# Kernel tuning notes

Hardware: AMD Instinct MI355X
Metric: run time of the kernel (lower is better)

The kernel has to match this reference:

```python
import jax, jax.numpy as jnp
import numpy as np

D = 1024
POOL_SIZES = [1024, 512, 256, 128, 64]  # n_pos=32*32 -> n_codes=64
CODEBOOK_SIZE = 512
BATCH = 32
W_SCALE = 0.03125  # ~1/sqrt(D) so pre-softmax logits stay O(1)


def setup_inputs() -> dict:
    key = jax.random.key(0)
    ks = jax.random.split(key, 7)
    x = jax.random.normal(ks[0], (BATCH, POOL_SIZES[0], D), dtype=jnp.float32)
    queries = jax.random.normal(ks[1], (len(POOL_SIZES), POOL_SIZES[0], D), dtype=jnp.float32)
    wq = jax.random.normal(ks[2], (len(POOL_SIZES), D, D), dtype=jnp.float32) * W_SCALE
    wk = jax.random.normal(ks[3], (len(POOL_SIZES), D, D), dtype=jnp.float32) * W_SCALE
    wv = jax.random.normal(ks[4], (len(POOL_SIZES), D, D), dtype=jnp.float32) * W_SCALE
    wo = jax.random.normal(ks[5], (len(POOL_SIZES), D, D), dtype=jnp.float32) * W_SCALE
    codebook = jax.random.normal(ks[6], (CODEBOOK_SIZE, D), dtype=jnp.float32)
    return {"x": x, "queries": queries, "wq": wq, "wk": wk, "wv": wv, "wo": wo, "codebook": codebook}


def reference(x, queries, wq, wk, wv, wo, codebook):
    # StackedPooling: S -> 1024 -> 512 -> 256 -> 128 -> 64 via AttentionPool stages
    scale = D ** (-0.5)
    h = x
    for i, K in enumerate(POOL_SIZES):
        q = queries[i, :K, :] @ wq[i]              # [K, D] learned queries, q_proj
        k = jnp.einsum("bsd,de->bse", h, wk[i])    # [B, S, D]
        v = jnp.einsum("bsd,de->bse", h, wv[i])    # [B, S, D]
        logits = jnp.einsum("kd,bsd->bks", q, k) * scale
        attn = jax.nn.softmax(logits, axis=-1)     # [B, K, S]
        pooled = jnp.einsum("bks,bsd->bkd", attn, v)
        h = jnp.einsum("bkd,de->bke", pooled, wo[i])  # [B, K, D]
    # VQ codebook quantization: nearest code per latent (squared L2)
    z = h                                          # [B, n_codes, D]
    d2 = (jnp.sum(z * z, axis=-1, keepdims=True)
          - 2.0 * jnp.einsum("bkd,cd->bkc", z, codebook)
          + jnp.sum(codebook * codebook, axis=-1))  # [B, n_codes, C]
    idx = jnp.argmin(d2, axis=-1)                  # [B, n_codes] int
    z_q = codebook[idx]                            # [B, n_codes, D]
    # straight-through estimator
    out = z + jax.lax.stop_gradient(z_q - z)
    return out
```

## Files before the change

### kernel.cpp

```cpp
#include <hip/hip_runtime.h>


#define MB (1024ull * 1024ull)

typedef unsigned short u16;
typedef __attribute__((ext_vector_type(4))) float f32x4;
typedef __bf16 bf16x8 __attribute__((ext_vector_type(8)));

__device__ __forceinline__ u16 f2bf(float f) {
  unsigned u = __float_as_uint(f);
  unsigned r = u + 0x7FFFu + ((u >> 16) & 1u);
  return (u16)(r >> 16);
}
__device__ __forceinline__ float bf2f(u16 h) {
  return __uint_as_float(((unsigned)h) << 16);
}

typedef __attribute__((address_space(1))) const void GASV;
typedef __attribute__((address_space(3))) void LASV;
__device__ __forceinline__ void async16(const void* g, void* l) {
  __builtin_amdgcn_global_load_lds((GASV*)g, (LASV*)l, 16, 0, 0);
}

__device__ __forceinline__ int xcd_swz(int bid, int nwg) {
  const int q8 = nwg >> 3, r8 = nwg & 7;
  const int xcd = bid & 7, idx = bid >> 3;
  return (xcd < r8 ? xcd * (q8 + 1) : r8 * (q8 + 1) + (xcd - r8) * q8) + idx;
}

template<int MODE>
__global__ __launch_bounds__(512, 1)
void gemm_c(const u16* __restrict__ A, const u16* __restrict__ B,
            float* __restrict__ Cf, u16* __restrict__ Cb,
            int M, int N, int KLEN, int ld,
            long long sA, long long sB, long long sC, int ldc, float alpha,
            int nxt, int nyt)
{
  __shared__ u16 lds[65536];
  const int tid  = threadIdx.x;
  const int lane = tid & 63;
  const int w    = tid >> 6;
  const int wr   = w >> 2, wc = w & 3;

  const int wg = xcd_swz((int)blockIdx.x, (int)gridDim.x);
  const int bx = wg % nxt;
  const int by = (wg / nxt) % nyt;
  const int bz = wg / (nxt * nyt);

  const int m0 = by * 256, n0 = bx * 256;
  const u16* Ab = A + (size_t)bz * sA;
  const u16* Bb = B + (size_t)bz * sB;
  const int NT = KLEN >> 6;

  f32x4 acc[8][4] = {};

  const int Rl  = tid >> 2;
  const int sgs = (tid & 3) ^ ((tid >> 3) & 3);
  int ra0 = m0 + Rl;        ra0 = ra0 < M - 1 ? ra0 : M - 1;
  int ra1 = m0 + 128 + Rl;  ra1 = ra1 < M - 1 ? ra1 : M - 1;
  int rb0 = n0 + Rl;        rb0 = rb0 < N - 1 ? rb0 : N - 1;
  int rb1 = n0 + 128 + Rl;  rb1 = rb1 < N - 1 ? rb1 : N - 1;
  const u16* gA0 = Ab + (size_t)ra0 * ld + (sgs << 3);
  const u16* gA1 = Ab + (size_t)ra1 * ld + (sgs << 3);
  const u16* gB0 = Bb + (size_t)rb0 * ld + (sgs << 3);
  const u16* gB1 = Bb + (size_t)rb1 * ld + (sgs << 3);
  const int ldst = (w << 4) * 32;

  auto stageH = [&](int mat, int buf, int kh, int tile) {
    const int tt = tile < NT ? tile : NT - 1;
    const int kc = (tt << 6) + (kh << 5);
    u16* d = &lds[(mat << 15) + (buf << 14) + (kh << 13) + ldst];
    if (mat == 0) {
      async16(gA0 + kc, d);
      async16(gA1 + kc, d + 4096);
    } else {
      async16(gB0 + kc, d);
      async16(gB1 + kc, d + 4096);
    }
  };

  const int rsel = lane & 15;
  const int ksub = lane >> 4;
  const int sw   = ksub ^ ((rsel >> 1) & 3);
  const u16* ldsA = &lds[(wr * 128 + rsel) * 32 + sw * 8];
  const u16* ldsB = &lds[32768 + (wc * 64 + rsel) * 32 + sw * 8];

  auto phase = [&](int buf, int kh, int mh, bf16x8* b,
                   int smat, int sbuf, int skh, int stile, int vm) {
    bf16x8 a[4];
    if (mh == 0) {
#pragma unroll
      for (int ni = 0; ni < 4; ++ni)
        b[ni] = *(const bf16x8*)&ldsB[buf * 16384 + kh * 8192 + ni * 512];
    }
#pragma unroll
    for (int mi = 0; mi < 4; ++mi)
      a[mi] = *(const bf16x8*)&ldsA[buf * 16384 + kh * 8192 + mh * 2048 + mi * 512];
    stageH(smat, sbuf, skh, stile);
    if (vm == 10)     asm volatile("s_waitcnt vmcnt(10)" ::: "memory");
    else if (vm == 6) asm volatile("s_waitcnt vmcnt(6)" ::: "memory");
    __builtin_amdgcn_s_barrier();
    asm volatile("s_waitcnt lgkmcnt(0)" ::: "memory");
    __builtin_amdgcn_sched_barrier(0);
    __builtin_amdgcn_s_setprio(1);
#pragma unroll
    for (int mi = 0; mi < 4; ++mi)
#pragma unroll
      for (int ni = 0; ni < 4; ++ni)
        acc[mh * 4 + mi][ni] = __builtin_amdgcn_mfma_f32_16x16x32_bf16(
            a[mi], b[ni], acc[mh * 4 + mi][ni], 0, 0, 0);
    __builtin_amdgcn_s_setprio(0);
    __builtin_amdgcn_s_barrier();
  };

  stageH(1, 0, 0, 0); stageH(0, 0, 0, 0); stageH(1, 0, 1, 0); stageH(0, 0, 1, 0);
  stageH(1, 1, 0, 1); stageH(0, 1, 0, 1); stageH(1, 1, 1, 1);
  asm volatile("s_waitcnt vmcnt(6)" ::: "memory");
  __builtin_amdgcn_s_barrier();

  const int NI = NT >> 1;
  for (int it = 0; it < NI; ++it) {
    const int t0 = it << 1, t1 = t0 + 1;
    bf16x8 b0[4], b1[4];
    phase(0, 0, 0, b0, 0, 1, 1, t1,     -1);
    phase(0, 0, 1, b0, 1, 0, 0, t0 + 2, -1);
    phase(0, 1, 0, b1, 0, 0, 0, t0 + 2, -1);
    phase(0, 1, 1, b1, 1, 0, 1, t0 + 2, 10);
    phase(1, 0, 0, b0, 0, 0, 1, t0 + 2, -1);
    phase(1, 0, 1, b0, 1, 1, 0, t1 + 2, 10);
    phase(1, 1, 0, b1, 0, 1, 0, t1 + 2, -1);
    phase(1, 1, 1, b1, 1, 1, 1, t1 + 2, 6);
  }
  asm volatile("s_waitcnt vmcnt(0)" ::: "memory");

#pragma unroll
  for (int mi = 0; mi < 8; ++mi)
#pragma unroll
    for (int ni = 0; ni < 4; ++ni)
#pragma unroll
      for (int i = 0; i < 4; ++i) {
        const int row = m0 + wr * 128 + mi * 16 + ((lane >> 4) << 2) + i;
        const int col = n0 + wc * 64 + ni * 16 + rsel;
        if (row < M && col < N) {
          const float v = acc[mi][ni][i] * alpha;
          const size_t off = (size_t)bz * sC + (size_t)row * ldc + col;
          if (MODE == 0) Cf[off] = v;
          else           Cb[off] = f2bf(v);
        }
      }
}

template<int MODE>
__global__ __launch_bounds__(256, 2)
void gemm_s(const u16* __restrict__ A, const u16* __restrict__ B,
            float* __restrict__ Cf, u16* __restrict__ Cb,
            int M, int N, int KLEN, int ld,
            long long sA, long long sB, long long sC, int ldc, float alpha,
            int nxt, int nyt)
{
  __shared__ u16 lds[32768];
  const int tid  = threadIdx.x;
  const int lane = tid & 63;
  const int w    = tid >> 6;
  const int wr   = w >> 1, wc = w & 1;

  const int wg = xcd_swz((int)blockIdx.x, (int)gridDim.x);
  const int bx = wg % nxt;
  const int by = (wg / nxt) % nyt;
  const int bz = wg / (nxt * nyt);

  const int m0 = by * 128, n0 = bx * 128;
  const u16* Ab = A + (size_t)bz * sA;
  const u16* Bb = B + (size_t)bz * sB;
  const int NT = KLEN >> 6;

  f32x4 acc[4][4] = {};

  const int Rl  = tid >> 3;
  const int sgs = (tid & 7) ^ (Rl & 7);
  const int ldst = (w << 3) * 64;

  auto stage = [&](int t, int buf) {
    const int kc = t << 6;
#pragma unroll
    for (int mat = 0; mat < 2; ++mat)
#pragma unroll
      for (int j = 0; j < 4; ++j) {
        int rg = (mat ? n0 : m0) + j * 32 + Rl;
        const int lim = (mat ? N : M) - 1;
        rg = rg < lim ? rg : lim;
        const u16* src = (mat ? Bb : Ab) + (size_t)rg * ld + kc + (sgs << 3);
        async16(src, &lds[(buf << 14) + (mat << 13) + j * 2048 + ldst]);
      }
  };

  const int rsel = lane & 15, ksub = lane >> 4;
  const int e  = rsel & 7;
  const int s0 = ((e >> 2) << 2) | (ksub ^ (e & 3));
  const int s1 = s0 ^ 4;
  const u16* ldsA0 = &lds[(wr * 64 + rsel) * 64 + s0 * 8];
  const u16* ldsA1 = &lds[(wr * 64 + rsel) * 64 + s1 * 8];
  const u16* ldsB0 = &lds[8192 + (wc * 64 + rsel) * 64 + s0 * 8];
  const u16* ldsB1 = &lds[8192 + (wc * 64 + rsel) * 64 + s1 * 8];

  stage(0, 0);
  for (int t = 0; t < NT; ++t) {
    const int buf = t & 1;
    if (t + 1 < NT) {
      stage(t + 1, buf ^ 1);
      asm volatile("s_waitcnt vmcnt(8)" ::: "memory");
    } else {
      asm volatile("s_waitcnt vmcnt(0)" ::: "memory");
    }
    __builtin_amdgcn_s_barrier();
    bf16x8 af[4][2], bf[4][2];
#pragma unroll
    for (int f = 0; f < 4; ++f) {
      af[f][0] = *(const bf16x8*)&ldsA0[buf * 16384 + f * 1024];
      af[f][1] = *(const bf16x8*)&ldsA1[buf * 16384 + f * 1024];
      bf[f][0] = *(const bf16x8*)&ldsB0[buf * 16384 + f * 1024];
      bf[f][1] = *(const bf16x8*)&ldsB1[buf * 16384 + f * 1024];
    }
    asm volatile("s_waitcnt lgkmcnt(0)" ::: "memory");
    __builtin_amdgcn_sched_barrier(0);
    __builtin_amdgcn_s_setprio(1);
#pragma unroll
    for (int mi = 0; mi < 4; ++mi)
#pragma unroll
      for (int ni = 0; ni < 4; ++ni)
#pragma unroll
        for (int kh = 0; kh < 2; ++kh)
          acc[mi][ni] = __builtin_amdgcn_mfma_f32_16x16x32_bf16(
              af[mi][kh], bf[ni][kh], acc[mi][ni], 0, 0, 0);
    __builtin_amdgcn_s_setprio(0);
    __builtin_amdgcn_s_barrier();
  }

#pragma unroll
  for (int mi = 0; mi < 4; ++mi)
#pragma unroll
    for (int ni = 0; ni < 4; ++ni)
#pragma unroll
      for (int i = 0; i < 4; ++i) {
        const int row = m0 + wr * 64 + mi * 16 + ((lane >> 4) << 2) + i;
        const int col = n0 + wc * 64 + ni * 16 + rsel;
        if (row < M && col < N) {
          const float v = acc[mi][ni][i] * alpha;
          const size_t off = (size_t)bz * sC + (size_t)row * ldc + col;
          if (MODE == 0) Cf[off] = v;
          else           Cb[off] = f2bf(v);
        }
      }
}

__global__ void cast_k(const float* __restrict__ in, u16* __restrict__ out,
                       long long n4)
{
  long long i = (long long)blockIdx.x * 256 + threadIdx.x;
  const long long stride = (long long)gridDim.x * 256;
  for (; i < n4; i += stride) {
    const float4 v = *(const float4*)&in[i << 2];
    *(ushort4*)&out[i << 2] = make_ushort4(f2bf(v.x), f2bf(v.y), f2bf(v.z), f2bf(v.w));
  }
}

__global__ __launch_bounds__(256)
void cast_trans_k(const float* __restrict__ in, u16* __restrict__ h,
                  u16* __restrict__ ht)
{
  __shared__ float t[32][33];
  const int z = blockIdx.z;
  const float* src = in + (size_t)z * 1048576;
  u16* dh = h  + (size_t)z * 1048576;
  u16* dt = ht + (size_t)z * 1048576;
  const int x0 = blockIdx.x * 32, y0 = blockIdx.y * 32;
  const int tx = threadIdx.x, ty = threadIdx.y;
#pragma unroll
  for (int k = 0; k < 4; ++k) {
    const float v = src[(size_t)(y0 + ty + 8 * k) * 1024 + (x0 + tx)];
    t[ty + 8 * k][tx] = v;
    dh[(size_t)(y0 + ty + 8 * k) * 1024 + (x0 + tx)] = f2bf(v);
  }
  __syncthreads();
#pragma unroll
  for (int k = 0; k < 4; ++k)
    dt[(size_t)(x0 + ty + 8 * k) * 1024 + (y0 + tx)] = f2bf(t[tx][ty + 8 * k]);
}

__global__ __launch_bounds__(256)
void transpose_cast_k(const float* __restrict__ in, u16* __restrict__ out)
{
  __shared__ float t[32][33];
  const int z = blockIdx.z;
  const float* src = in + (size_t)z * 1048576;
  u16* dst = out + (size_t)z * 1048576;
  const int x0 = blockIdx.x * 32, y0 = blockIdx.y * 32;
  const int tx = threadIdx.x, ty = threadIdx.y;
#pragma unroll
  for (int k = 0; k < 4; ++k)
    t[ty + 8 * k][tx] = src[(size_t)(y0 + ty + 8 * k) * 1024 + (x0 + tx)];
  __syncthreads();
#pragma unroll
  for (int k = 0; k < 4; ++k)
    dst[(size_t)(x0 + ty + 8 * k) * 1024 + (y0 + tx)] = f2bf(t[tx][ty + 8 * k]);
}

__global__ __launch_bounds__(256)
void transpose_u16_k(const u16* __restrict__ in, u16* __restrict__ out, int R)
{
  __shared__ u16 t[32][33];
  const size_t zi = (size_t)blockIdx.z * R * 1024;
  const size_t zo = (size_t)blockIdx.z * 1024 * R;
  const int x0 = blockIdx.x * 32, y0 = blockIdx.y * 32;
  const int tx = threadIdx.x, ty = threadIdx.y;
#pragma unroll
  for (int k = 0; k < 4; ++k)
    t[ty + 8 * k][tx] = in[zi + (size_t)(y0 + ty + 8 * k) * 1024 + (x0 + tx)];
  __syncthreads();
#pragma unroll
  for (int k = 0; k < 4; ++k)
    out[zo + (size_t)(x0 + ty + 8 * k) * R + (y0 + tx)] = t[tx][ty + 8 * k];
}

__global__ __launch_bounds__(256)
void softmax_b(const u16* __restrict__ lg, u16* __restrict__ at, int S)
{
  const size_t row = blockIdx.x;
  const u16* src = lg + row * S;
  const int tid = threadIdx.x;
  float v[4];
  float mx = -3.402823466e38f;
#pragma unroll
  for (int c = 0; c < 4; ++c) {
    const int j = tid + c * 256;
    v[c] = (j < S) ? bf2f(src[j]) : -3.402823466e38f;
    mx = fmaxf(mx, v[c]);
  }
#pragma unroll
  for (int o = 32; o > 0; o >>= 1) mx = fmaxf(mx, __shfl_xor(mx, o));
  __shared__ float rmx[4];
  if ((tid & 63) == 0) rmx[tid >> 6] = mx;
  __syncthreads();
  mx = fmaxf(fmaxf(rmx[0], rmx[1]), fmaxf(rmx[2], rmx[3]));
  float sum = 0.f;
#pragma unroll
  for (int c = 0; c < 4; ++c) { v[c] = expf(v[c] - mx); sum += v[c]; }
#pragma unroll
  for (int o = 32; o > 0; o >>= 1) sum += __shfl_xor(sum, o);
  __shared__ float rsm[4];
  if ((tid & 63) == 0) rsm[tid >> 6] = sum;
  __syncthreads();
  sum = rsm[0] + rsm[1] + rsm[2] + rsm[3];
  const float inv = 1.0f / sum;
  u16* dst = at + row * S;
#pragma unroll
  for (int c = 0; c < 4; ++c) {
    const int j = tid + c * 256;
    if (j < S) dst[j] = f2bf(v[c] * inv);
  }
}

__global__ __launch_bounds__(256)
void cnorm_kernel(const float* __restrict__ cb, float* __restrict__ cn)
{
  const int c = blockIdx.x;
  const float4 v = ((const float4*)(cb + (size_t)c * 1024))[threadIdx.x];
  float s = v.x * v.x + v.y * v.y + v.z * v.z + v.w * v.w;
#pragma unroll
  for (int o = 32; o > 0; o >>= 1) s += __shfl_xor(s, o);
  __shared__ float r4[4];
  if ((threadIdx.x & 63) == 0) r4[threadIdx.x >> 6] = s;
  __syncthreads();
  if (threadIdx.x == 0) cn[c] = r4[0] + r4[1] + r4[2] + r4[3];
}

__global__ __launch_bounds__(256)
void argmin_gather_k(const float* __restrict__ dot, const float* __restrict__ cn,
                     const float* __restrict__ cb, float* __restrict__ out)
{
  const size_t lat = blockIdx.x;
  const int tid = threadIdx.x;
  float best = 3.402823466e38f;
  int bi = 0;
#pragma unroll
  for (int cc = 0; cc < 2; ++cc) {
    const int c = tid + cc * 256;
    float d = 0.f;
#pragma unroll
    for (int p = 0; p < 4; ++p) d += dot[(size_t)p * 1048576 + lat * 512 + c];
    const float sc = cn[c] - 2.0f * d;
    if (sc < best || (sc == best && c < bi)) { best = sc; bi = c; }
  }
  __shared__ float rb[256];
  __shared__ int   ri[256];
  rb[tid] = best; ri[tid] = bi;
  __syncthreads();
  for (int s = 128; s > 0; s >>= 1) {
    if (tid < s) {
      const float ob = rb[tid + s];
      const int oi = ri[tid + s];
      if (ob < rb[tid] || (ob == rb[tid] && oi < ri[tid])) { rb[tid] = ob; ri[tid] = oi; }
    }
    __syncthreads();
  }
  const int sel = ri[0];
  ((float4*)(out + lat * 1024))[tid] = ((const float4*)(cb + (size_t)sel * 1024))[tid];
}

__global__ void fill_kernel(float* p, float v, int n) {
  const int i = blockIdx.x * 256 + threadIdx.x;
  if (i < n) p[i] = v;
}

static void gX(hipStream_t st, int mode,
               const u16* A, const u16* B, float* Cf, u16* Cb,
               int M, int N, int KLEN, int ld,
               long long sA, long long sB, long long sC, int ldc,
               int batch, float alpha)
{
  const int b256 = ((M + 255) / 256) * ((N + 255) / 256) * batch;
  if (b256 >= 192 && (KLEN & 127) == 0) {
    const int nxt = (N + 255) / 256, nyt = (M + 255) / 256;
    dim3 grid(nxt * nyt * batch), blk(512);
    if (mode == 0)
      gemm_c<0><<<grid, blk, 0, st>>>(A, B, Cf, Cb, M, N, KLEN, ld, sA, sB, sC, ldc, alpha, nxt, nyt);
    else
      gemm_c<1><<<grid, blk, 0, st>>>(A, B, Cf, Cb, M, N, KLEN, ld, sA, sB, sC, ldc, alpha, nxt, nyt);
  } else {
    const int nxt = (N + 127) / 128, nyt = (M + 127) / 128;
    dim3 grid(nxt * nyt * batch), blk(256);
    if (mode == 0)
      gemm_s<0><<<grid, blk, 0, st>>>(A, B, Cf, Cb, M, N, KLEN, ld, sA, sB, sC, ldc, alpha, nxt, nyt);
    else
      gemm_s<1><<<grid, blk, 0, st>>>(A, B, Cf, Cb, M, N, KLEN, ld, sA, sB, sC, ldc, alpha, nxt, nyt);
  }
}

extern "C" void kernel_launch(void* const* d_in, const int* in_sizes, int n_in,
                              void* d_out, int out_size, void* d_ws, size_t ws_size,
                              hipStream_t stream)
{
  const float* x   = (const float*)d_in[0];
  const float* qry = (const float*)d_in[1];
  const float* wq  = (const float*)d_in[2];
  const float* wk  = (const float*)d_in[3];
  const float* wv  = (const float*)d_in[4];
  const float* wo  = (const float*)d_in[5];
  const float* cb  = (const float*)d_in[6];
  float* out = (float*)d_out;

  const size_t NEED = 298 * MB;
  if (ws_size < NEED) {
    fill_kernel<<<(out_size + 255) / 256, 256, 0, stream>>>(out, (float)ws_size, out_size);
    return;
  }
  char* ws = (char*)d_ws;
  const long long W = 1048576;
  u16*  QKb  = (u16*)(ws + 0 * MB);
  u16*  WVOb = (u16*)(ws + 10 * MB);
  u16*  CBb  = (u16*)(ws + 20 * MB);
  float* CN  = (float*)(ws + 21 * MB);
  u16*  Zb   = (u16*)(ws + 22 * MB);
  float* DOT = (float*)(ws + 26 * MB);
  u16*  Hb   = (u16*)(ws + 42 * MB);
  u16*  HTb  = (u16*)(ws + 106 * MB);
  u16*  ATb  = (u16*)(ws + 170 * MB);
  u16*  LOG  = (u16*)(ws + 234 * MB);
  u16*  Mb   = (u16*)(ws + 234 * MB);
  u16*  QSb   = (u16*)(ws + 42 * MB);
  u16*  WQb   = (u16*)(ws + 52 * MB);
  u16*  WKb   = (u16*)(ws + 62 * MB);
  u16*  WVb   = (u16*)(ws + 72 * MB);
  u16*  WOTb  = (u16*)(ws + 82 * MB);
  u16*  WqkTb = (u16*)(ws + 92 * MB);

  const int S_in[5]  = {1024, 1024, 512, 256, 128};
  const int K_out[5] = {1024, 512, 256, 128, 64};

  cast_k<<<2048, 256, 0, stream>>>(qry, QSb, 1310720ll);
  cast_k<<<2048, 256, 0, stream>>>(wq, WQb, 1310720ll);
  cast_k<<<2048, 256, 0, stream>>>(wk, WKb, 1310720ll);
  cast_k<<<2048, 256, 0, stream>>>(wv, WVb, 1310720ll);
  cast_k<<<512, 256, 0, stream>>>(cb, CBb, 131072ll);
  dim3 tb(32, 8), tg5(32, 32, 5);
  transpose_cast_k<<<tg5, tb, 0, stream>>>(wo, WOTb);
  cnorm_kernel<<<512, 256, 0, stream>>>(cb, CN);

  gX(stream, 1, WKb, WQb, nullptr, WqkTb, 1024, 1024, 1024, 1024, W, W, W, 1024, 5, 1.0f);
  gX(stream, 1, QSb, WqkTb, nullptr, QKb, 1024, 1024, 1024, 1024, W, W, W, 1024, 5, 1.0f);
  gX(stream, 1, WOTb, WVb, nullptr, WVOb, 1024, 1024, 1024, 1024, W, W, W, 1024, 5, 1.0f);

  dim3 tgx(32, 32, 32);
  cast_trans_k<<<tgx, tb, 0, stream>>>(x, Hb, HTb);

  for (int i = 0; i < 5; ++i) {
    const int S = S_in[i], KO = K_out[i];

    gX(stream, 1, QKb + (size_t)i * W, Hb, nullptr, LOG,
       KO, S, 1024, 1024, 0, (long long)S * 1024, (long long)KO * S, S, 32, 0.03125f);
    softmax_b<<<32 * KO, 256, 0, stream>>>(LOG, ATb, S);
    gX(stream, 1, ATb, HTb, nullptr, Mb,
       KO, 1024, S, S, (long long)KO * S, (long long)1024 * S, (long long)KO * 1024, 1024, 32, 1.0f);
    if (i < 4) {
      gX(stream, 1, Mb, WVOb + (size_t)i * W, nullptr, Hb,
         32 * KO, 1024, 1024, 1024, 0, 0, 0, 1024, 1, 1.0f);
      dim3 tgt(32, KO / 32, 32);
      transpose_u16_k<<<tgt, tb, 0, stream>>>(Hb, HTb, KO);
    } else {
      gX(stream, 1, Mb, WVOb + (size_t)i * W, nullptr, Zb,
         32 * KO, 1024, 1024, 1024, 0, 0, 0, 1024, 1, 1.0f);
    }
  }

  gX(stream, 0, Zb, CBb, DOT, nullptr,
     2048, 512, 256, 1024, 256, 256, (long long)2048 * 512, 512, 4, 1.0f);
  argmin_gather_k<<<2048, 256, 0, stream>>>(DOT, CN, cb, out);
}
```

Measured before the change: 772.3 us.

## Fold per-stage value/output projections into query and codebook weight products

Result: faster. 733.1 us (-5.1%).

```diff
diff --git a/kernel.cpp b/kernel.cpp
--- a/kernel.cpp
+++ b/kernel.cpp
@@ -70,13 +70,8 @@
     const int tt = tile < NT ? tile : NT - 1;
     const int kc = (tt << 6) + (kh << 5);
     u16* d = &lds[(mat << 15) + (buf << 14) + (kh << 13) + ldst];
-    if (mat == 0) {
-      async16(gA0 + kc, d);
-      async16(gA1 + kc, d + 4096);
-    } else {
-      async16(gB0 + kc, d);
-      async16(gB1 + kc, d + 4096);
-    }
+    if (mat == 0) { async16(gA0 + kc, d); async16(gA1 + kc, d + 4096); }
+    else          { async16(gB0 + kc, d); async16(gB1 + kc, d + 4096); }
   };
 
   const int rsel = lane & 15;
@@ -380,15 +375,13 @@
 {
   const size_t lat = blockIdx.x;
   const int tid = threadIdx.x;
+  const float* dr = dot + lat * 512;
   float best = 3.402823466e38f;
   int bi = 0;
 #pragma unroll
   for (int cc = 0; cc < 2; ++cc) {
     const int c = tid + cc * 256;
-    float d = 0.f;
-#pragma unroll
-    for (int p = 0; p < 4; ++p) d += dot[(size_t)p * 1048576 + lat * 512 + c];
-    const float sc = cn[c] - 2.0f * d;
+    const float sc = cn[c] - 2.0f * dr[c];
     if (sc < best || (sc == best && c < bi)) { best = sc; bi = c; }
   }
   __shared__ float rb[256];
@@ -412,14 +405,15 @@
   if (i < n) p[i] = v;
 }
 
-static void gX(hipStream_t st, int mode,
+static void gX(hipStream_t st, int mode, int force,
                const u16* A, const u16* B, float* Cf, u16* Cb,
                int M, int N, int KLEN, int ld,
                long long sA, long long sB, long long sC, int ldc,
                int batch, float alpha)
 {
   const int b256 = ((M + 255) / 256) * ((N + 255) / 256) * batch;
-  if (b256 >= 192 && (KLEN & 127) == 0) {
+  const bool big = (force == 2) || (force == 0 && b256 >= 192 && (KLEN & 127) == 0);
+  if (big) {
     const int nxt = (N + 255) / 256, nyt = (M + 255) / 256;
     dim3 grid(nxt * nyt * batch), blk(512);
     if (mode == 0)
@@ -449,7 +443,7 @@
   const float* cb  = (const float*)d_in[6];
   float* out = (float*)d_out;
 
-  const size_t NEED = 298 * MB;
+  const size_t NEED = 312 * MB;
   if (ws_size < NEED) {
     fill_kernel<<<(out_size + 255) / 256, 256, 0, stream>>>(out, (float)ws_size, out_size);
     return;
@@ -458,21 +452,24 @@
   const long long W = 1048576;
   u16*  QKb  = (u16*)(ws + 0 * MB);
   u16*  WVOb = (u16*)(ws + 10 * MB);
-  u16*  CBb  = (u16*)(ws + 20 * MB);
-  float* CN  = (float*)(ws + 21 * MB);
-  u16*  Zb   = (u16*)(ws + 22 * MB);
-  float* DOT = (float*)(ws + 26 * MB);
-  u16*  Hb   = (u16*)(ws + 42 * MB);
-  u16*  HTb  = (u16*)(ws + 106 * MB);
-  u16*  ATb  = (u16*)(ws + 170 * MB);
-  u16*  LOG  = (u16*)(ws + 234 * MB);
-  u16*  Mb   = (u16*)(ws + 234 * MB);
-  u16*  QSb   = (u16*)(ws + 42 * MB);
-  u16*  WQb   = (u16*)(ws + 52 * MB);
-  u16*  WKb   = (u16*)(ws + 62 * MB);
-  u16*  WVb   = (u16*)(ws + 72 * MB);
-  u16*  WOTb  = (u16*)(ws + 82 * MB);
-  u16*  WqkTb = (u16*)(ws + 92 * MB);
+  u16*  WVOs = (u16*)(ws + 20 * MB);
+  u16*  CBb  = (u16*)(ws + 30 * MB);
+  float* CN  = (float*)(ws + 31 * MB);
+  u16*  QKP  = (u16*)(ws + 32 * MB);
+  u16*  WCb  = (u16*)(ws + 40 * MB);
+  u16*  WC5  = (u16*)(ws + 48 * MB);
+  u16*  CBW  = (u16*)(ws + 50 * MB);
+  float* DOT = (float*)(ws + 51 * MB);
+  u16*  U    = (u16*)(ws + 56 * MB);
+  u16*  UT   = (u16*)(ws + 120 * MB);
+  u16*  ATb  = (u16*)(ws + 184 * MB);
+  u16*  LOG  = (u16*)(ws + 248 * MB);
+  u16*  QSb   = (u16*)(ws + 56 * MB);
+  u16*  WQb   = (u16*)(ws + 66 * MB);
+  u16*  WKb   = (u16*)(ws + 76 * MB);
+  u16*  WVb   = (u16*)(ws + 86 * MB);
+  u16*  WOTb  = (u16*)(ws + 96 * MB);
+  u16*  WqkTb = (u16*)(ws + 106 * MB);
 
   const int S_in[5]  = {1024, 1024, 512, 256, 128};
   const int K_out[5] = {1024, 512, 256, 128, 64};
@@ -486,33 +483,38 @@
   transpose_cast_k<<<tg5, tb, 0, stream>>>(wo, WOTb);
   cnorm_kernel<<<512, 256, 0, stream>>>(cb, CN);
 
-  gX(stream, 1, WKb, WQb, nullptr, WqkTb, 1024, 1024, 1024, 1024, W, W, W, 1024, 5, 1.0f);
-  gX(stream, 1, QSb, WqkTb, nullptr, QKb, 1024, 1024, 1024, 1024, W, W, W, 1024, 5, 1.0f);
-  gX(stream, 1, WOTb, WVb, nullptr, WVOb, 1024, 1024, 1024, 1024, W, W, W, 1024, 5, 1.0f);
+  gX(stream, 1, 0, WKb, WQb, nullptr, WqkTb, 1024, 1024, 1024, 1024, W, W, W, 1024, 5, 1.0f);
+  gX(stream, 1, 0, QSb, WqkTb, nullptr, QKb, 1024, 1024, 1024, 1024, W, W, W, 1024, 5, 1.0f);
+  gX(stream, 1, 0, WOTb, WVb, nullptr, WVOb, 1024, 1024, 1024, 1024, W, W, W, 1024, 5, 1.0f);
+  gX(stream, 1, 0, WVb, WOTb, nullptr, WVOs, 1024, 1024, 1024, 1024, W, W, W, 1024, 5, 1.0f);
+
+  hipMemcpyAsync(WCb, WVOs, 2 * MB, hipMemcpyDeviceToDevice, stream);
+  gX(stream, 1, 0, WCb,         WVOb + 1 * W, nullptr, WCb + 1 * W, 1024, 1024, 1024, 1024, 0, 0, 0, 1024, 1, 1.0f);
+  gX(stream, 1, 0, WCb + 1 * W, WVOb + 2 * W, nullptr, WCb + 2 * W, 1024, 1024, 1024, 1024, 0, 0, 0, 1024, 1, 1.0f);
+  gX(stream, 1, 0, WCb + 2 * W, WVOb + 3 * W, nullptr, WCb + 3 * W, 1024, 1024, 1024, 1024, 0, 0, 0, 1024, 1, 1.0f);
+  gX(stream, 1, 0, WCb + 3 * W, WVOb + 4 * W, nullptr, WC5,         1024, 1024, 1024, 1024, 0, 0, 0, 1024, 1, 1.0f);
+  gX(stream, 1, 0, QKb + W, WCb, nullptr, QKP, 1024, 1024, 1024, 1024, W, W, W, 1024, 4, 1.0f);
+  gX(stream, 1, 0, CBb, WC5, nullptr, CBW, 512, 1024, 1024, 1024, 0, 0, 0, 1024, 1, 1.0f);
 
   dim3 tgx(32, 32, 32);
-  cast_trans_k<<<tgx, tb, 0, stream>>>(x, Hb, HTb);
+  cast_trans_k<<<tgx, tb, 0, stream>>>(x, U, UT);
 
   for (int i = 0; i < 5; ++i) {
     const int S = S_in[i], KO = K_out[i];
-
-    gX(stream, 1, QKb + (size_t)i * W, Hb, nullptr, LOG,
+    const u16* qk = (i == 0) ? QKb : QKP + (size_t)(i - 1) * W;
+
+    gX(stream, 1, (i == 0) ? 1 : 0, qk, U, nullptr, LOG,
        KO, S, 1024, 1024, 0, (long long)S * 1024, (long long)KO * S, S, 32, 0.03125f);
     softmax_b<<<32 * KO, 256, 0, stream>>>(LOG, ATb, S);
-    gX(stream, 1, ATb, HTb, nullptr, Mb,
+    gX(stream, 1, (i == 0) ? 2 : 0, ATb, UT, nullptr, U,
        KO, 1024, S, S, (long long)KO * S, (long long)1024 * S, (long long)KO * 1024, 1024, 32, 1.0f);
     if (i < 4) {
-      gX(stream, 1, Mb, WVOb + (size_t)i * W, nullptr, Hb,
-         32 * KO, 1024, 1024, 1024, 0, 0, 0, 1024, 1, 1.0f);
       dim3 tgt(32, KO / 32, 32);
-      transpose_u16_k<<<tgt, tb, 0, stream>>>(Hb, HTb, KO);
-    } else {
-      gX(stream, 1, Mb, WVOb + (size_t)i * W, nullptr, Zb,
-         32 * KO, 1024, 1024, 1024, 0, 0, 0, 1024, 1, 1.0f);
+      transpose_u16_k<<<tgt, tb, 0, stream>>>(U, UT, KO);
     }
   }
 
-  gX(stream, 0, Zb, CBb, DOT, nullptr,
-     2048, 512, 256, 1024, 256, 256, (long long)2048 * 512, 512, 4, 1.0f);
+  gX(stream, 0, 0, U, CBW, DOT, nullptr,
+     2048, 512, 1024, 1024, 0, 0, 0, 512, 1, 1.0f);
   argmin_gather_k<<<2048, 256, 0, stream>>>(DOT, CN, cb, out);
 }
```
